# Kernel tuning notes

Hardware: AMD Instinct MI355X
Metric: run time of the kernel (lower is better)

The kernel has to match this reference:

```python
import jax, jax.numpy as jnp
from jax import lax
import numpy as np

IN, H, OUT, G = 1, 32, 30, 4 * 32  # input_size, hidden_size, output_size, gate dim


def _lstm_layer(x_tbd, Wih, Whh, bih, bhh):
    # x_tbd: [T, B, D_in]; torch gate order: i, f, g, o
    B = x_tbd.shape[1]
    h0 = jnp.zeros((B, H), x_tbd.dtype)
    c0 = jnp.zeros((B, H), x_tbd.dtype)

    def step(carry, xt):
        h, c = carry
        z = xt @ Wih.T + h @ Whh.T + (bih + bhh)  # [B, 4H]
        i, f, g, o = jnp.split(z, 4, axis=-1)
        c = jax.nn.sigmoid(f) * c + jax.nn.sigmoid(i) * jnp.tanh(g)
        h = jax.nn.sigmoid(o) * jnp.tanh(c)
        return (h, c), h

    (hT, cT), hs = lax.scan(step, (h0, c0), x_tbd)
    return hs, hT


def setup_inputs() -> dict:
    key = jax.random.key(0)
    ks = jax.random.split(key, 16)
    B, T = 4096, 512
    s = 1.0 / np.sqrt(H)  # torch LSTM init scale
    inp = {"x": jax.random.normal(ks[0], (B, T, IN), dtype=jnp.float32)}
    for l, din in enumerate([IN, H, H]):
        inp[f"Wih{l}"] = jax.random.uniform(ks[1 + 4 * l], (G, din), jnp.float32, -s, s)
        inp[f"Whh{l}"] = jax.random.uniform(ks[2 + 4 * l], (G, H), jnp.float32, -s, s)
        inp[f"bih{l}"] = jax.random.uniform(ks[3 + 4 * l], (G,), jnp.float32, -s, s)
        inp[f"bhh{l}"] = jax.random.uniform(ks[4 + 4 * l], (G,), jnp.float32, -s, s)
    inp["W2"] = jax.random.uniform(ks[13], (OUT, H), jnp.float32, -s, s)
    inp["b2"] = jax.random.uniform(ks[14], (OUT,), jnp.float32, -s, s)
    return inp


def reference(x, Wih0, Whh0, bih0, bhh0, Wih1, Whh1, bih1, bhh1,
              Wih2, Whh2, bih2, bhh2, W2, b2):
    # batch_first input -> time-major for scan
    xt = jnp.transpose(x, (1, 0, 2))  # [T, B, IN]
    hs, _ = _lstm_layer(xt, Wih0, Whh0, bih0, bhh0)
    hs, _ = _lstm_layer(hs, Wih1, Whh1, bih1, bhh1)
    _, h_last = _lstm_layer(hs, Wih2, Whh2, bih2, bhh2)  # h[-1]: [B, H]
    return h_last @ W2.T + b2  # [B, OUT]
```

## Files before the change

### kernel.cpp

```cpp
#include <hip/hip_runtime.h>
#include <cstdint>
#include <cstddef>

#define TT   512
#define MT   16
#define OUTN 30

typedef __attribute__((ext_vector_type(8))) short short8;
typedef __attribute__((ext_vector_type(4))) float floatx4;

static __device__ __forceinline__ float fast_sigmoid(float x) {
    float e = __builtin_amdgcn_exp2f(-1.4426950408889634f * x);
    return __builtin_amdgcn_rcpf(1.0f + e);
}
static __device__ __forceinline__ float fast_tanh(float x) {
    float e = __builtin_amdgcn_exp2f(-2.8853900817779268f * x);
    return 2.0f * __builtin_amdgcn_rcpf(1.0f + e) - 1.0f;
}
static __device__ __forceinline__ unsigned short to_bf16(float f) {
    union { float f; unsigned int u; } v; v.f = f;
    return (unsigned short)((v.u + 0x7FFFu + ((v.u >> 16) & 1u)) >> 16);
}

static __device__ __forceinline__ short8 load_frag_perm(const float* __restrict__ W, int arow, int k0) {
    int orig = (arow & 3) * 32 + (arow >> 2);
    const float* p = W + orig * 32 + k0;
    short8 s;
#pragma unroll
    for (int e = 0; e < 8; ++e) s[e] = (short)to_bf16(p[e]);
    return s;
}
static __device__ __forceinline__ short8 load_frag_plain(const float* __restrict__ W, int row, int k0) {
    const float* p = W + row * 32 + k0;
    short8 s;
#pragma unroll
    for (int e = 0; e < 8; ++e) s[e] = (short)to_bf16(p[e]);
    return s;
}

__global__ __launch_bounds__(512, 2) void lstm_fused(
    const float* __restrict__ x,
    const float* __restrict__ Wih0, const float* __restrict__ Whh0,
    const float* __restrict__ bih0, const float* __restrict__ bhh0,
    const float* __restrict__ Wih1, const float* __restrict__ Whh1,
    const float* __restrict__ bih1, const float* __restrict__ bhh1,
    const float* __restrict__ Wih2, const float* __restrict__ Whh2,
    const float* __restrict__ bih2, const float* __restrict__ bhh2,
    const float* __restrict__ W2,   const float* __restrict__ b2,
    float* __restrict__ out)
{
    __shared__ float xs[MT][TT + 4];
    __shared__ unsigned short h0s[2][4][MT][8];
    __shared__ unsigned short h1s[2][4][MT][8];
    __shared__ unsigned short h2s[2][4][MT][8];

    const int tid  = (int)threadIdx.x;
    const int wv   = tid >> 6;
    const int l    = tid & 63;
    const int b    = l & 15;
    const int q    = l >> 4;
    const int u    = 4 * wv + q;
    const int uc   = u >> 3, ue = u & 7;
    const int bt   = (int)blockIdx.x;
    const int arow = 16 * wv + b;
    const int k0   = q * 8;

    {
        const floatx4* xg = (const floatx4*)(x + (size_t)bt * MT * TT);
#pragma unroll
        for (int j = 0; j < 4; ++j) {
            int idx = tid + j * 512;
            int row = idx >> 7;
            int c4  = idx & 127;
            *(floatx4*)&xs[row][c4 * 4] = xg[idx];
        }
    }
    {
        unsigned short* p0 = (unsigned short*)h0s;
        unsigned short* p1 = (unsigned short*)h1s;
        unsigned short* p2 = (unsigned short*)h2s;
        for (int i = tid; i < 2 * 4 * MT * 8; i += 512) { p0[i] = 0; p1[i] = 0; p2[i] = 0; }
    }

    short8 whh0f = load_frag_perm(Whh0, arow, k0);
    short8 wih1f = load_frag_perm(Wih1, arow, k0);
    short8 whh1f = load_frag_perm(Whh1, arow, k0);
    short8 wih2f = load_frag_perm(Wih2, arow, k0);
    short8 whh2f = load_frag_perm(Whh2, arow, k0);

    float wx0[4], bz0[4], bz1[4], bz2[4];
#pragma unroll
    for (int r = 0; r < 4; ++r) {
        int idx = r * 32 + u;
        wx0[r] = Wih0[idx];
        bz0[r] = bih0[idx] + bhh0[idx];
        bz1[r] = bih1[idx] + bhh1[idx];
        bz2[r] = bih2[idx] + bhh2[idx];
    }

    short8 w2f = {};
    float b2v[4] = {0.f, 0.f, 0.f, 0.f};
    if (wv < 2) {
        int r2 = 16 * wv + b;
        int rc = r2 < OUTN ? r2 : OUTN - 1;
        w2f = load_frag_plain(W2, rc, k0);
#pragma unroll
        for (int r = 0; r < 4; ++r) {
            int rr = 16 * wv + 4 * q + r;
            b2v[r] = (rr < OUTN) ? b2[rr] : 0.0f;
        }
    }

    float c0 = 0.f, c1 = 0.f, c2 = 0.f;
    const floatx4 zero4 = {0.f, 0.f, 0.f, 0.f};

    __syncthreads();

    {
        float xv = xs[b][0];
        float i0 = fast_sigmoid(xv * wx0[0] + bz0[0]);
        float g0 = fast_tanh   (xv * wx0[2] + bz0[2]);
        float o0 = fast_sigmoid(xv * wx0[3] + bz0[3]);
        c0 = i0 * g0;
        h0s[0][uc][b][ue] = to_bf16(o0 * fast_tanh(c0));
        __syncthreads();
    }
    {
        short8 bh0 = *(const short8*)&h0s[0][q][b][0];
        floatx4 z0 = __builtin_amdgcn_mfma_f32_16x16x32_bf16(whh0f, bh0, zero4, 0, 0, 0);
        floatx4 z1 = __builtin_amdgcn_mfma_f32_16x16x32_bf16(wih1f, bh0, zero4, 0, 0, 0);
        float xv = xs[b][1];
        float i0 = fast_sigmoid(z0[0] + xv * wx0[0] + bz0[0]);
        float f0 = fast_sigmoid(z0[1] + xv * wx0[1] + bz0[1]);
        float g0 = fast_tanh   (z0[2] + xv * wx0[2] + bz0[2]);
        float o0 = fast_sigmoid(z0[3] + xv * wx0[3] + bz0[3]);
        c0 = f0 * c0 + i0 * g0;
        unsigned short h0b = to_bf16(o0 * fast_tanh(c0));
        float i1 = fast_sigmoid(z1[0] + bz1[0]);
        float g1 = fast_tanh   (z1[2] + bz1[2]);
        float o1 = fast_sigmoid(z1[3] + bz1[3]);
        c1 = i1 * g1;
        unsigned short h1b = to_bf16(o1 * fast_tanh(c1));
        h0s[1][uc][b][ue] = h0b;
        h1s[1][uc][b][ue] = h1b;
        __syncthreads();
    }

    auto STEP = [&](int t0, int wb) {
        const int rb = wb ^ 1;
        short8 bh0 = *(const short8*)&h0s[rb][q][b][0];
        short8 bh1 = *(const short8*)&h1s[rb][q][b][0];
        short8 bh2 = *(const short8*)&h2s[rb][q][b][0];
        floatx4 z0 = __builtin_amdgcn_mfma_f32_16x16x32_bf16(whh0f, bh0, zero4, 0, 0, 0);
        floatx4 z1 = __builtin_amdgcn_mfma_f32_16x16x32_bf16(whh1f, bh1, zero4, 0, 0, 0);
        floatx4 z2 = __builtin_amdgcn_mfma_f32_16x16x32_bf16(whh2f, bh2, zero4, 0, 0, 0);
        z1 = __builtin_amdgcn_mfma_f32_16x16x32_bf16(wih1f, bh0, z1, 0, 0, 0);
        z2 = __builtin_amdgcn_mfma_f32_16x16x32_bf16(wih2f, bh1, z2, 0, 0, 0);
        float xv = xs[b][t0];
        float i0 = fast_sigmoid(z0[0] + xv * wx0[0] + bz0[0]);
        float f0 = fast_sigmoid(z0[1] + xv * wx0[1] + bz0[1]);
        float g0 = fast_tanh   (z0[2] + xv * wx0[2] + bz0[2]);
        float o0 = fast_sigmoid(z0[3] + xv * wx0[3] + bz0[3]);
        c0 = f0 * c0 + i0 * g0;
        unsigned short h0b = to_bf16(o0 * fast_tanh(c0));
        float i1 = fast_sigmoid(z1[0] + bz1[0]);
        float f1 = fast_sigmoid(z1[1] + bz1[1]);
        float g1 = fast_tanh   (z1[2] + bz1[2]);
        float o1 = fast_sigmoid(z1[3] + bz1[3]);
        c1 = f1 * c1 + i1 * g1;
        unsigned short h1b = to_bf16(o1 * fast_tanh(c1));
        float i2 = fast_sigmoid(z2[0] + bz2[0]);
        float f2 = fast_sigmoid(z2[1] + bz2[1]);
        float g2 = fast_tanh   (z2[2] + bz2[2]);
        float o2 = fast_sigmoid(z2[3] + bz2[3]);
        c2 = f2 * c2 + i2 * g2;
        unsigned short h2b = to_bf16(o2 * fast_tanh(c2));
        h0s[wb][uc][b][ue] = h0b;
        h1s[wb][uc][b][ue] = h1b;
        h2s[wb][uc][b][ue] = h2b;
        __syncthreads();
    };
    for (int k = 2; k < TT; k += 2) { STEP(k, 0); STEP(k + 1, 1); }

    {
        short8 bh0 = *(const short8*)&h0s[1][q][b][0];
        short8 bh1 = *(const short8*)&h1s[1][q][b][0];
        short8 bh2 = *(const short8*)&h2s[1][q][b][0];
        floatx4 z1 = __builtin_amdgcn_mfma_f32_16x16x32_bf16(whh1f, bh1, zero4, 0, 0, 0);
        floatx4 z2 = __builtin_amdgcn_mfma_f32_16x16x32_bf16(whh2f, bh2, zero4, 0, 0, 0);
        z1 = __builtin_amdgcn_mfma_f32_16x16x32_bf16(wih1f, bh0, z1, 0, 0, 0);
        z2 = __builtin_amdgcn_mfma_f32_16x16x32_bf16(wih2f, bh1, z2, 0, 0, 0);
        float i1 = fast_sigmoid(z1[0] + bz1[0]);
        float f1 = fast_sigmoid(z1[1] + bz1[1]);
        float g1 = fast_tanh   (z1[2] + bz1[2]);
        float o1 = fast_sigmoid(z1[3] + bz1[3]);
        c1 = f1 * c1 + i1 * g1;
        unsigned short h1b = to_bf16(o1 * fast_tanh(c1));
        float i2 = fast_sigmoid(z2[0] + bz2[0]);
        float f2 = fast_sigmoid(z2[1] + bz2[1]);
        float g2 = fast_tanh   (z2[2] + bz2[2]);
        float o2 = fast_sigmoid(z2[3] + bz2[3]);
        c2 = f2 * c2 + i2 * g2;
        unsigned short h2b = to_bf16(o2 * fast_tanh(c2));
        h1s[0][uc][b][ue] = h1b;
        h2s[0][uc][b][ue] = h2b;
        __syncthreads();
    }
    {
        short8 bh1 = *(const short8*)&h1s[0][q][b][0];
        short8 bh2 = *(const short8*)&h2s[0][q][b][0];
        floatx4 z2 = __builtin_amdgcn_mfma_f32_16x16x32_bf16(whh2f, bh2, zero4, 0, 0, 0);
        z2 = __builtin_amdgcn_mfma_f32_16x16x32_bf16(wih2f, bh1, z2, 0, 0, 0);
        float i2 = fast_sigmoid(z2[0] + bz2[0]);
        float f2 = fast_sigmoid(z2[1] + bz2[1]);
        float g2 = fast_tanh   (z2[2] + bz2[2]);
        float o2 = fast_sigmoid(z2[3] + bz2[3]);
        c2 = f2 * c2 + i2 * g2;
        h2s[1][uc][b][ue] = to_bf16(o2 * fast_tanh(c2));
        __syncthreads();
    }

    if (wv < 2) {
        short8 bh2 = *(const short8*)&h2s[1][q][b][0];
        floatx4 zo = __builtin_amdgcn_mfma_f32_16x16x32_bf16(w2f, bh2, zero4, 0, 0, 0);
#pragma unroll
        for (int r = 0; r < 4; ++r) {
            int rr = 16 * wv + 4 * q + r;
            if (rr < OUTN)
                out[(size_t)(bt * MT + b) * OUTN + rr] = zo[r] + b2v[r];
        }
    }
}

extern "C" void kernel_launch(void* const* d_in, const int* in_sizes, int n_in,
                              void* d_out, int out_size, void* d_ws, size_t ws_size,
                              hipStream_t stream) {
    const float* x    = (const float*)d_in[0];
    const float* Wih0 = (const float*)d_in[1];
    const float* Whh0 = (const float*)d_in[2];
    const float* bih0 = (const float*)d_in[3];
    const float* bhh0 = (const float*)d_in[4];
    const float* Wih1 = (const float*)d_in[5];
    const float* Whh1 = (const float*)d_in[6];
    const float* bih1 = (const float*)d_in[7];
    const float* bhh1 = (const float*)d_in[8];
    const float* Wih2 = (const float*)d_in[9];
    const float* Whh2 = (const float*)d_in[10];
    const float* bih2 = (const float*)d_in[11];
    const float* bhh2 = (const float*)d_in[12];
    const float* W2   = (const float*)d_in[13];
    const float* b2   = (const float*)d_in[14];
    float* out = (float*)d_out;

    dim3 grid(4096 / MT);
    dim3 block(512);
    hipLaunchKernelGGL(lstm_fused, grid, block, 0, stream,
                       x, Wih0, Whh0, bih0, bhh0,
                       Wih1, Whh1, bih1, bhh1,
                       Wih2, Whh2, bih2, bhh2, W2, b2, out);
}
```

Before: 283.9 us.

## Fold gate scales into weights, share reciprocals, seed MFMA accumulators with bias

Pre-multiplies weights and biases by the exp2 scale factors, so each gate needs a single exp2 with no separate multiply. Sigmoid pairs now share one reciprocal each, and the tanh(c) step is folded into an FMA. Biases and the x-input term are passed as the MFMA accumulator, removing the adds after the matrix op, and the 0-init of h2 is replaced by a peeled third step. It also switches to hardware bf16 conversion and reads x four steps at a time. Multiplying two denominators before the reciprocal risks overflow to infinity for large negative pre-activations, which can change results.

```diff
diff --git a/kernel.cpp b/kernel.cpp
--- a/kernel.cpp
+++ b/kernel.cpp
@@ -9,33 +9,59 @@
 typedef __attribute__((ext_vector_type(8))) short short8;
 typedef __attribute__((ext_vector_type(4))) float floatx4;
 
-static __device__ __forceinline__ float fast_sigmoid(float x) {
-    float e = __builtin_amdgcn_exp2f(-1.4426950408889634f * x);
-    return __builtin_amdgcn_rcpf(1.0f + e);
-}
-static __device__ __forceinline__ float fast_tanh(float x) {
-    float e = __builtin_amdgcn_exp2f(-2.8853900817779268f * x);
-    return 2.0f * __builtin_amdgcn_rcpf(1.0f + e) - 1.0f;
+#define NLOG2E  (-1.4426950408889634f)
+#define N2LOG2E (-2.8853900817779268f)
+
+static __device__ __forceinline__ float rcpf(float x) { return __builtin_amdgcn_rcpf(x); }
+static __device__ __forceinline__ float ex2(float x)  { return __builtin_amdgcn_exp2f(x); }
+
+static __device__ __forceinline__ unsigned short cvt_bf16(float f) {
+    unsigned int r;
+    asm("v_cvt_pk_bf16_f32 %0, %1, %2" : "=v"(r) : "v"(f), "v"(f));
+    return (unsigned short)r;
 }
 static __device__ __forceinline__ unsigned short to_bf16(float f) {
     union { float f; unsigned int u; } v; v.f = f;
     return (unsigned short)((v.u + 0x7FFFu + ((v.u >> 16) & 1u)) >> 16);
 }
 
+static __device__ __forceinline__ float gate_scale(int gate) {
+    return (gate == 2) ? N2LOG2E : NLOG2E;
+}
+
 static __device__ __forceinline__ short8 load_frag_perm(const float* __restrict__ W, int arow, int k0) {
-    int orig = (arow & 3) * 32 + (arow >> 2);
+    int gate = arow & 3;
+    int orig = gate * 32 + (arow >> 2);
+    float s = gate_scale(gate);
     const float* p = W + orig * 32 + k0;
-    short8 s;
-#pragma unroll
-    for (int e = 0; e < 8; ++e) s[e] = (short)to_bf16(p[e]);
-    return s;
+    short8 v;
+#pragma unroll
+    for (int e = 0; e < 8; ++e) v[e] = (short)to_bf16(s * p[e]);
+    return v;
 }
 static __device__ __forceinline__ short8 load_frag_plain(const float* __restrict__ W, int row, int k0) {
     const float* p = W + row * 32 + k0;
-    short8 s;
-#pragma unroll
-    for (int e = 0; e < 8; ++e) s[e] = (short)to_bf16(p[e]);
-    return s;
+    short8 v;
+#pragma unroll
+    for (int e = 0; e < 8; ++e) v[e] = (short)to_bf16(p[e]);
+    return v;
+}
+
+static __device__ __forceinline__ unsigned short lstm_gates(floatx4 z, float& c) {
+    float Di = 1.0f + ex2(z[0]);
+    float Df = 1.0f + ex2(z[1]);
+    float Dg = 1.0f + ex2(z[2]);
+    float Do = 1.0f + ex2(z[3]);
+    float rif = rcpf(Di * Df);
+    float i = Df * rif;
+    float f = Di * rif;
+    float rgo = rcpf(Dg * Do);
+    float g = __builtin_fmaf(2.0f, Do * rgo, -1.0f);
+    float o = Dg * rgo;
+    c = __builtin_fmaf(f, c, i * g);
+    float tc = rcpf(1.0f + ex2(N2LOG2E * c));
+    float h = __builtin_fmaf(o + o, tc, -o);
+    return cvt_bf16(h);
 }
 
 __global__ __launch_bounds__(512, 2) void lstm_fused(
@@ -75,12 +101,6 @@
             *(floatx4*)&xs[row][c4 * 4] = xg[idx];
         }
     }
-    {
-        unsigned short* p0 = (unsigned short*)h0s;
-        unsigned short* p1 = (unsigned short*)h1s;
-        unsigned short* p2 = (unsigned short*)h2s;
-        for (int i = tid; i < 2 * 4 * MT * 8; i += 512) { p0[i] = 0; p1[i] = 0; p2[i] = 0; }
-    }
 
     short8 whh0f = load_frag_perm(Whh0, arow, k0);
     short8 wih1f = load_frag_perm(Wih1, arow, k0);
@@ -88,18 +108,20 @@
     short8 wih2f = load_frag_perm(Wih2, arow, k0);
     short8 whh2f = load_frag_perm(Whh2, arow, k0);
 
-    float wx0[4], bz0[4], bz1[4], bz2[4];
+    float wx0[4];
+    floatx4 bc0, bc1, bc2;
 #pragma unroll
     for (int r = 0; r < 4; ++r) {
         int idx = r * 32 + u;
-        wx0[r] = Wih0[idx];
-        bz0[r] = bih0[idx] + bhh0[idx];
-        bz1[r] = bih1[idx] + bhh1[idx];
-        bz2[r] = bih2[idx] + bhh2[idx];
+        float s = gate_scale(r);
+        wx0[r] = s * Wih0[idx];
+        bc0[r] = s * (bih0[idx] + bhh0[idx]);
+        bc1[r] = s * (bih1[idx] + bhh1[idx]);
+        bc2[r] = s * (bih2[idx] + bhh2[idx]);
     }
 
     short8 w2f = {};
-    float b2v[4] = {0.f, 0.f, 0.f, 0.f};
+    floatx4 b2c = {0.f, 0.f, 0.f, 0.f};
     if (wv < 2) {
         int r2 = 16 * wv + b;
         int rc = r2 < OUTN ? r2 : OUTN - 1;
@@ -107,101 +129,91 @@
 #pragma unroll
         for (int r = 0; r < 4; ++r) {
             int rr = 16 * wv + 4 * q + r;
-            b2v[r] = (rr < OUTN) ? b2[rr] : 0.0f;
+            b2c[r] = (rr < OUTN) ? b2[rr] : 0.0f;
         }
     }
 
     float c0 = 0.f, c1 = 0.f, c2 = 0.f;
-    const floatx4 zero4 = {0.f, 0.f, 0.f, 0.f};
 
     __syncthreads();
 
-    {
-        float xv = xs[b][0];
-        float i0 = fast_sigmoid(xv * wx0[0] + bz0[0]);
-        float g0 = fast_tanh   (xv * wx0[2] + bz0[2]);
-        float o0 = fast_sigmoid(xv * wx0[3] + bz0[3]);
-        c0 = i0 * g0;
-        h0s[0][uc][b][ue] = to_bf16(o0 * fast_tanh(c0));
+    auto bc0x = [&](float xv) {
+        floatx4 c4v;
+#pragma unroll
+        for (int r = 0; r < 4; ++r) c4v[r] = __builtin_fmaf(xv, wx0[r], bc0[r]);
+        return c4v;
+    };
+
+    {
+        floatx4 z0 = bc0x(xs[b][0]);
+        h0s[0][uc][b][ue] = lstm_gates(z0, c0);
         __syncthreads();
     }
     {
         short8 bh0 = *(const short8*)&h0s[0][q][b][0];
-        floatx4 z0 = __builtin_amdgcn_mfma_f32_16x16x32_bf16(whh0f, bh0, zero4, 0, 0, 0);
-        floatx4 z1 = __builtin_amdgcn_mfma_f32_16x16x32_bf16(wih1f, bh0, zero4, 0, 0, 0);
-        float xv = xs[b][1];
-        float i0 = fast_sigmoid(z0[0] + xv * wx0[0] + bz0[0]);
-        float f0 = fast_sigmoid(z0[1] + xv * wx0[1] + bz0[1]);
-        float g0 = fast_tanh   (z0[2] + xv * wx0[2] + bz0[2]);
-        float o0 = fast_sigmoid(z0[3] + xv * wx0[3] + bz0[3]);
-        c0 = f0 * c0 + i0 * g0;
-        unsigned short h0b = to_bf16(o0 * fast_tanh(c0));
-        float i1 = fast_sigmoid(z1[0] + bz1[0]);
-        float g1 = fast_tanh   (z1[2] + bz1[2]);
-        float o1 = fast_sigmoid(z1[3] + bz1[3]);
-        c1 = i1 * g1;
-        unsigned short h1b = to_bf16(o1 * fast_tanh(c1));
+        floatx4 z0 = __builtin_amdgcn_mfma_f32_16x16x32_bf16(whh0f, bh0, bc0x(xs[b][1]), 0, 0, 0);
+        floatx4 z1 = __builtin_amdgcn_mfma_f32_16x16x32_bf16(wih1f, bh0, bc1, 0, 0, 0);
+        unsigned short h0b = lstm_gates(z0, c0);
+        unsigned short h1b = lstm_gates(z1, c1);
         h0s[1][uc][b][ue] = h0b;
         h1s[1][uc][b][ue] = h1b;
         __syncthreads();
     }
-
-    auto STEP = [&](int t0, int wb) {
+    {
+        short8 bh0 = *(const short8*)&h0s[1][q][b][0];
+        short8 bh1 = *(const short8*)&h1s[1][q][b][0];
+        floatx4 z0 = __builtin_amdgcn_mfma_f32_16x16x32_bf16(whh0f, bh0, bc0x(xs[b][2]), 0, 0, 0);
+        floatx4 z1 = __builtin_amdgcn_mfma_f32_16x16x32_bf16(whh1f, bh1, bc1, 0, 0, 0);
+        z1 = __builtin_amdgcn_mfma_f32_16x16x32_bf16(wih1f, bh0, z1, 0, 0, 0);
+        floatx4 z2 = __builtin_amdgcn_mfma_f32_16x16x32_bf16(wih2f, bh1, bc2, 0, 0, 0);
+        unsigned short h0b = lstm_gates(z0, c0);
+        unsigned short h1b = lstm_gates(z1, c1);
+        unsigned short h2b = lstm_gates(z2, c2);
+        h0s[0][uc][b][ue] = h0b;
+        h1s[0][uc][b][ue] = h1b;
+        h2s[0][uc][b][ue] = h2b;
+        __syncthreads();
+    }
+
+    auto STEP = [&](float xv, int wb) {
         const int rb = wb ^ 1;
         short8 bh0 = *(const short8*)&h0s[rb][q][b][0];
         short8 bh1 = *(const short8*)&h1s[rb][q][b][0];
         short8 bh2 = *(const short8*)&h2s[rb][q][b][0];
-        floatx4 z0 = __builtin_amdgcn_mfma_f32_16x16x32_bf16(whh0f, bh0, zero4, 0, 0, 0);
-        floatx4 z1 = __builtin_amdgcn_mfma_f32_16x16x32_bf16(whh1f, bh1, zero4, 0, 0, 0);
-        floatx4 z2 = __builtin_amdgcn_mfma_f32_16x16x32_bf16(whh2f, bh2, zero4, 0, 0, 0);
+        floatx4 z0 = __builtin_amdgcn_mfma_f32_16x16x32_bf16(whh0f, bh0, bc0x(xv), 0, 0, 0);
+        floatx4 z1 = __builtin_amdgcn_mfma_f32_16x16x32_bf16(whh1f, bh1, bc1, 0, 0, 0);
+        floatx4 z2 = __builtin_amdgcn_mfma_f32_16x16x32_bf16(whh2f, bh2, bc2, 0, 0, 0);
         z1 = __builtin_amdgcn_mfma_f32_16x16x32_bf16(wih1f, bh0, z1, 0, 0, 0);
         z2 = __builtin_amdgcn_mfma_f32_16x16x32_bf16(wih2f, bh1, z2, 0, 0, 0);
-        float xv = xs[b][t0];
-        float i0 = fast_sigmoid(z0[0] + xv * wx0[0] + bz0[0]);
-        float f0 = fast_sigmoid(z0[1] + xv * wx0[1] + bz0[1]);
-        float g0 = fast_tanh   (z0[2] + xv * wx0[2] + bz0[2]);
-        float o0 = fast_sigmoid(z0[3] + xv * wx0[3] + bz0[3]);
-        c0 = f0 * c0 + i0 * g0;
-        unsigned short h0b = to_bf16(o0 * fast_tanh(c0));
-        float i1 = fast_sigmoid(z1[0] + bz1[0]);
-        float f1 = fast_sigmoid(z1[1] + bz1[1]);
-        float g1 = fast_tanh   (z1[2] + bz1[2]);
-        float o1 = fast_sigmoid(z1[3] + bz1[3]);
-        c1 = f1 * c1 + i1 * g1;
-        unsigned short h1b = to_bf16(o1 * fast_tanh(c1));
-        float i2 = fast_sigmoid(z2[0] + bz2[0]);
-        float f2 = fast_sigmoid(z2[1] + bz2[1]);
-        float g2 = fast_tanh   (z2[2] + bz2[2]);
-        float o2 = fast_sigmoid(z2[3] + bz2[3]);
-        c2 = f2 * c2 + i2 * g2;
-        unsigned short h2b = to_bf16(o2 * fast_tanh(c2));
+        unsigned short h0b = lstm_gates(z0, c0);
+        unsigned short h1b = lstm_gates(z1, c1);
+        unsigned short h2b = lstm_gates(z2, c2);
         h0s[wb][uc][b][ue] = h0b;
         h1s[wb][uc][b][ue] = h1b;
         h2s[wb][uc][b][ue] = h2b;
         __syncthreads();
     };
-    for (int k = 2; k < TT; k += 2) { STEP(k, 0); STEP(k + 1, 1); }
+
+    STEP(xs[b][3], 1);
+
+    for (int k = 4; k < TT; k += 4) {
+        floatx4 xq = *(const floatx4*)&xs[b][k];
+        STEP(xq[0], 0);
+        STEP(xq[1], 1);
+        STEP(xq[2], 0);
+        STEP(xq[3], 1);
+    }
 
     {
         short8 bh0 = *(const short8*)&h0s[1][q][b][0];
         short8 bh1 = *(const short8*)&h1s[1][q][b][0];
         short8 bh2 = *(const short8*)&h2s[1][q][b][0];
-        floatx4 z1 = __builtin_amdgcn_mfma_f32_16x16x32_bf16(whh1f, bh1, zero4, 0, 0, 0);
-        floatx4 z2 = __builtin_amdgcn_mfma_f32_16x16x32_bf16(whh2f, bh2, zero4, 0, 0, 0);
+        floatx4 z1 = __builtin_amdgcn_mfma_f32_16x16x32_bf16(whh1f, bh1, bc1, 0, 0, 0);
         z1 = __builtin_amdgcn_mfma_f32_16x16x32_bf16(wih1f, bh0, z1, 0, 0, 0);
+        floatx4 z2 = __builtin_amdgcn_mfma_f32_16x16x32_bf16(whh2f, bh2, bc2, 0, 0, 0);
         z2 = __builtin_amdgcn_mfma_f32_16x16x32_bf16(wih2f, bh1, z2, 0, 0, 0);
-        float i1 = fast_sigmoid(z1[0] + bz1[0]);
-        float f1 = fast_sigmoid(z1[1] + bz1[1]);
-        float g1 = fast_tanh   (z1[2] + bz1[2]);
-        float o1 = fast_sigmoid(z1[3] + bz1[3]);
-        c1 = f1 * c1 + i1 * g1;
-        unsigned short h1b = to_bf16(o1 * fast_tanh(c1));
-        float i2 = fast_sigmoid(z2[0] + bz2[0]);
-        float f2 = fast_sigmoid(z2[1] + bz2[1]);
-        float g2 = fast_tanh   (z2[2] + bz2[2]);
-        float o2 = fast_sigmoid(z2[3] + bz2[3]);
-        c2 = f2 * c2 + i2 * g2;
-        unsigned short h2b = to_bf16(o2 * fast_tanh(c2));
+        unsigned short h1b = lstm_gates(z1, c1);
+        unsigned short h2b = lstm_gates(z2, c2);
         h1s[0][uc][b][ue] = h1b;
         h2s[0][uc][b][ue] = h2b;
         __syncthreads();
@@ -209,25 +221,20 @@
     {
         short8 bh1 = *(const short8*)&h1s[0][q][b][0];
         short8 bh2 = *(const short8*)&h2s[0][q][b][0];
-        floatx4 z2 = __builtin_amdgcn_mfma_f32_16x16x32_bf16(whh2f, bh2, zero4, 0, 0, 0);
+        floatx4 z2 = __builtin_amdgcn_mfma_f32_16x16x32_bf16(whh2f, bh2, bc2, 0, 0, 0);
         z2 = __builtin_amdgcn_mfma_f32_16x16x32_bf16(wih2f, bh1, z2, 0, 0, 0);
-        float i2 = fast_sigmoid(z2[0] + bz2[0]);
-        float f2 = fast_sigmoid(z2[1] + bz2[1]);
-        float g2 = fast_tanh   (z2[2] + bz2[2]);
-        float o2 = fast_sigmoid(z2[3] + bz2[3]);
-        c2 = f2 * c2 + i2 * g2;
-        h2s[1][uc][b][ue] = to_bf16(o2 * fast_tanh(c2));
+        h2s[1][uc][b][ue] = lstm_gates(z2, c2);
         __syncthreads();
     }
 
     if (wv < 2) {
         short8 bh2 = *(const short8*)&h2s[1][q][b][0];
-        floatx4 zo = __builtin_amdgcn_mfma_f32_16x16x32_bf16(w2f, bh2, zero4, 0, 0, 0);
+        floatx4 zo = __builtin_amdgcn_mfma_f32_16x16x32_bf16(w2f, bh2, b2c, 0, 0, 0);
 #pragma unroll
         for (int r = 0; r < 4; ++r) {
             int rr = 16 * wv + 4 * q + r;
             if (rr < OUTN)
-                out[(size_t)(bt * MT + b) * OUTN + rr] = zo[r] + b2v[r];
+                out[(size_t)(bt * MT + b) * OUTN + rr] = zo[r];
         }
     }
 }
```

Result: faster. 255.7 us (-9.9%).
